# Kernel tuning notes

Measured on AMD Instinct MI355X. Metric: run time of the kernel, lower is better.

Reference implementation:

```python
import jax, jax.numpy as jnp
import numpy as np

N = 50000
E = 800000
IN_C, HID_C, OUT_C = 128, 256, 128
BN_EPS = 1e-5


def glorot(key, shape):
    fan_in, fan_out = shape
    lim = float(np.sqrt(6.0 / (fan_in + fan_out)))
    return jax.random.uniform(key, shape, jnp.float32, -lim, lim)


def setup_inputs() -> dict:
    key = jax.random.key(0)
    ks = jax.random.split(key, 16)
    inp = {
        "x": jax.random.normal(ks[0], (N, IN_C), jnp.float32),
        "edge_index": jax.random.randint(ks[1], (2, E), 0, N, jnp.int64),
        # SAGEConv 1 (in->hid): lin_l has bias, lin_r has no bias (PyG default)
        "wl1": glorot(ks[2], (IN_C, HID_C)), "bl1": jnp.zeros((HID_C,), jnp.float32),
        "wr1": glorot(ks[3], (IN_C, HID_C)),
        # SAGEConv 2 (hid->hid)
        "wl2": glorot(ks[4], (HID_C, HID_C)), "bl2": jnp.zeros((HID_C,), jnp.float32),
        "wr2": glorot(ks[5], (HID_C, HID_C)),
        # SAGEConv 3 (hid->out)
        "wl3": glorot(ks[6], (HID_C, OUT_C)), "bl3": jnp.zeros((OUT_C,), jnp.float32),
        "wr3": glorot(ks[7], (HID_C, OUT_C)),
        # BatchNorm params (eval mode: running stats)
        "bn1_w": jnp.ones((HID_C,), jnp.float32), "bn1_b": jnp.zeros((HID_C,), jnp.float32),
        "bn1_m": jax.random.normal(ks[8], (HID_C,), jnp.float32) * 0.1,
        "bn1_v": jax.random.uniform(ks[9], (HID_C,), jnp.float32, 0.5, 1.5),
        "bn2_w": jnp.ones((HID_C,), jnp.float32), "bn2_b": jnp.zeros((HID_C,), jnp.float32),
        "bn2_m": jax.random.normal(ks[10], (HID_C,), jnp.float32) * 0.1,
        "bn2_v": jax.random.uniform(ks[11], (HID_C,), jnp.float32, 0.5, 1.5),
    }
    return inp


def sage_conv(x, src, dst, wl, bl, wr):
    # mean aggregation of source-node features at destination nodes
    agg = jax.ops.segment_sum(x[src], dst, num_segments=N)          # [N, d_in]
    deg = jax.ops.segment_sum(jnp.ones((E,), x.dtype), dst, num_segments=N)
    mean = agg / jnp.maximum(deg, 1.0)[:, None]
    return mean @ wl + bl + x @ wr                                   # [N, d_out]


def batch_norm(x, w, b, m, v):
    return (x - m) * jax.lax.rsqrt(v + BN_EPS) * w + b


def reference(x, edge_index, wl1, bl1, wr1, wl2, bl2, wr2, wl3, bl3, wr3,
              bn1_w, bn1_b, bn1_m, bn1_v, bn2_w, bn2_b, bn2_m, bn2_v):
    src, dst = edge_index[0], edge_index[1]
    # layer 1: SAGEConv -> BN -> ReLU (dropout is identity in eval mode)
    h = sage_conv(x, src, dst, wl1, bl1, wr1)
    h = jax.nn.relu(batch_norm(h, bn1_w, bn1_b, bn1_m, bn1_v))
    # layer 2
    h = sage_conv(h, src, dst, wl2, bl2, wr2)
    h = jax.nn.relu(batch_norm(h, bn2_w, bn2_b, bn2_m, bn2_v))
    # output layer: plain SAGEConv
    return sage_conv(h, src, dst, wl3, bl3, wr3)
```

## Files before the change

### kernel.cpp

```cpp
#include <hip/hip_runtime.h>
#include <hip/hip_bf16.h>

#define NN 50000
#define NE 800000
#define NSB 49
#define AGG_BLOCKS 2048

typedef __attribute__((ext_vector_type(8))) short bh8;
typedef __attribute__((ext_vector_type(4))) float f32x4;

static __device__ __forceinline__ unsigned short f2bf(float f){
  unsigned u = __float_as_uint(f);
  unsigned r = (u + 0x7fffu + ((u >> 16) & 1u)) >> 16;
  return (unsigned short)r;
}
static __device__ __forceinline__ float bflo(unsigned u){ return __uint_as_float(u << 16); }
static __device__ __forceinline__ float bfhi(unsigned u){ return __uint_as_float(u & 0xffff0000u); }
static __device__ __forceinline__ unsigned packbf2(float lo, float hi){
  return ((unsigned)f2bf(hi) << 16) | (unsigned)f2bf(lo);
}

static __device__ __forceinline__ void gload16(const void* g, void* l){
  __builtin_amdgcn_global_load_lds(
      (const __attribute__((address_space(1))) unsigned int*)g,
      (__attribute__((address_space(3))) unsigned int*)l, 16, 0, 0);
}

__global__ void hist_k(const int* __restrict__ dstv, int* __restrict__ cnt,
                       int* __restrict__ rank){
  int i = blockIdx.x * 256 + threadIdx.x;
  if (i < NE) rank[i] = atomicAdd(&cnt[dstv[i]], 1);
}

__global__ __launch_bounds__(256) void scan1_k(const int* __restrict__ cnt,
                                               int* __restrict__ rowp,
                                               int* __restrict__ bsum){
  __shared__ int sa[256], sb[256];
  const int t = threadIdx.x, blk = blockIdx.x;
  const int base = blk * 1024 + t * 4;
  int4 v = make_int4(0, 0, 0, 0);
  if (base + 3 < NN) v = *reinterpret_cast<const int4*>(cnt + base);
  else if (base < NN){
    v.x = cnt[base];
    if (base + 1 < NN) v.y = cnt[base + 1];
    if (base + 2 < NN) v.z = cnt[base + 2];
  }
  const int s = v.x + v.y + v.z + v.w;
  sa[t] = s; __syncthreads();
  int* a = sa; int* b = sb;
  for (int off = 1; off < 256; off <<= 1){
    int val = a[t]; if (t >= off) val += a[t - off];
    b[t] = val; __syncthreads();
    int* tmp = a; a = b; b = tmp;
  }
  const int ex = a[t] - s;
  if (base < NN){
    rowp[base] = ex;
    if (base + 1 < NN) rowp[base + 1] = ex + v.x;
    if (base + 2 < NN) rowp[base + 2] = ex + v.x + v.y;
    if (base + 3 < NN) rowp[base + 3] = ex + v.x + v.y + v.z;
  }
  if (t == 255) bsum[blk] = a[255];
}

__global__ void scan2_k(int* __restrict__ bsum){
  __shared__ int s[64];
  const int t = threadIdx.x;
  s[t] = (t < NSB) ? bsum[t] : 0;
  __syncthreads();
  if (t == 0){
    int run = 0;
    for (int i = 0; i < NSB; ++i){ int c = s[i]; s[i] = run; run += c; }
  }
  __syncthreads();
  if (t < NSB) bsum[t] = s[t];
}

__global__ __launch_bounds__(256) void scan3_k(int* __restrict__ rowp,
                                               const int* __restrict__ bsum){
  const int blk = blockIdx.x;
  const int base = blk * 1024 + threadIdx.x * 4;
  const int off = bsum[blk];
  #pragma unroll
  for (int i = 0; i < 4; ++i){
    int idx = base + i;
    if (idx < NN) rowp[idx] += off;
  }
  if (blk == 0 && threadIdx.x == 0) rowp[NN] = NE;
}

__global__ __launch_bounds__(256) void fill_k(const int* __restrict__ srcv,
                       const int* __restrict__ dstv,
                       const int* __restrict__ rank,
                       const int* __restrict__ rowp, int* __restrict__ csrc){
  const int part  = blockIdx.x & 7;
  const int chunk = blockIdx.x >> 3;
  const int lo = part * (NN / 8);
  const int hi = lo + (NN / 8);
  const int base = chunk * (NE / 128);
  const int endi = base + (NE / 128);
  for (int i = base + threadIdx.x; i < endi; i += 256){
    int d = dstv[i];
    if (d >= lo && d < hi){
      csrc[rowp[d] + rank[i]] = srcv[i];
    }
  }
}

__global__ void f2b_k(const float4* __restrict__ x, uint2* __restrict__ xb){
  int i = blockIdx.x * 256 + threadIdx.x;
  if (i < NN * 128 / 4){
    float4 v = x[i];
    uint2 o; o.x = packbf2(v.x, v.y); o.y = packbf2(v.z, v.w);
    xb[i] = o;
  }
}

__global__ void f8conv_k(const uint4* __restrict__ h1, uint2* __restrict__ h1q){
  int i = blockIdx.x * 256 + threadIdx.x;
  if (i < NN * 256 / 8){
    uint4 v = h1[i];
    float f0 = bflo(v.x), f1 = bfhi(v.x), f2 = bflo(v.y), f3 = bfhi(v.y);
    float f4 = bflo(v.z), f5 = bfhi(v.z), f6 = bflo(v.w), f7 = bfhi(v.w);
    int w0 = 0, w1 = 0;
    w0 = __builtin_amdgcn_cvt_pk_fp8_f32(f0, f1, w0, false);
    w0 = __builtin_amdgcn_cvt_pk_fp8_f32(f2, f3, w0, true);
    w1 = __builtin_amdgcn_cvt_pk_fp8_f32(f4, f5, w1, false);
    w1 = __builtin_amdgcn_cvt_pk_fp8_f32(f6, f7, w1, true);
    uint2 o; o.x = (unsigned)w0; o.y = (unsigned)w1;
    h1q[i] = o;
  }
}

__global__ void prep_k(const float* __restrict__ wl1, const float* __restrict__ wr1,
                       const float* __restrict__ wl2, const float* __restrict__ wr2,
                       const float* __restrict__ wl3, const float* __restrict__ wr3,
                       const float* __restrict__ bl1, const float* __restrict__ bl2,
                       const float* __restrict__ bn1w, const float* __restrict__ bn1b,
                       const float* __restrict__ bn1m, const float* __restrict__ bn1v,
                       const float* __restrict__ bn2w, const float* __restrict__ bn2b,
                       const float* __restrict__ bn2m, const float* __restrict__ bn2v,
                       unsigned short* __restrict__ B1t, unsigned short* __restrict__ B2t,
                       unsigned short* __restrict__ B3t,
                       float* __restrict__ S1, float* __restrict__ T1,
                       float* __restrict__ S2, float* __restrict__ T2){
  int i = blockIdx.x * 256 + threadIdx.x;
  if (i < 65536){
    int n = i >> 8, k = i & 255;
    float v = (k < 128) ? wl1[k * 256 + n] : wr1[(k - 128) * 256 + n];
    B1t[n * 256 + k] = f2bf(v);
  } else if (i < 65536 + 131072){
    int j = i - 65536; int n = j >> 9, k = j & 511;
    float v = (k < 256) ? wl2[k * 256 + n] : wr2[(k - 256) * 256 + n];
    B2t[n * 512 + k] = f2bf(v);
  } else if (i < 65536 + 131072 + 65536){
    int j = i - (65536 + 131072); int n = j >> 8, k = j & 255;
    float v = (n < 128) ? wl3[k * 128 + n] : wr3[k * 128 + (n - 128)];
    B3t[n * 256 + k] = f2bf(v);
  } else if (i < 65536 + 131072 + 65536 + 512){
    int j = i - (65536 + 131072 + 65536);
    if (j < 256){
      float s = bn1w[j] * rsqrtf(bn1v[j] + 1e-5f);
      S1[j] = s; T1[j] = (bl1[j] - bn1m[j]) * s + bn1b[j];
    } else {
      int c = j - 256;
      float s = bn2w[c] * rsqrtf(bn2v[c] + 1e-5f);
      S2[c] = s; T2[c] = (bl2[c] - bn2m[c]) * s + bn2b[c];
    }
  }
}

__global__ __launch_bounds__(256) void agg128_k(const unsigned* __restrict__ feat, unsigned* __restrict__ out,
                         const int* __restrict__ rowp, const int* __restrict__ csrc){
  const int lane = threadIdx.x & 63;
  const int node0 = __builtin_amdgcn_readfirstlane(blockIdx.x * 4 + (threadIdx.x >> 6));
  const int nw = gridDim.x * 4;
  for (int node = node0; node < NN; node += nw){
    const int start = rowp[node], end = rowp[node + 1];
    float a0 = 0.f, a1 = 0.f, b0 = 0.f, b1 = 0.f;
    int e = start;
    for (; e + 7 < end; e += 8){
      unsigned u0 = feat[(size_t)csrc[e]     * 64 + lane];
      unsigned u1 = feat[(size_t)csrc[e + 1] * 64 + lane];
      unsigned u2 = feat[(size_t)csrc[e + 2] * 64 + lane];
      unsigned u3 = feat[(size_t)csrc[e + 3] * 64 + lane];
      unsigned u4 = feat[(size_t)csrc[e + 4] * 64 + lane];
      unsigned u5 = feat[(size_t)csrc[e + 5] * 64 + lane];
      unsigned u6 = feat[(size_t)csrc[e + 6] * 64 + lane];
      unsigned u7 = feat[(size_t)csrc[e + 7] * 64 + lane];
      a0 += bflo(u0); a1 += bfhi(u0);
      b0 += bflo(u1); b1 += bfhi(u1);
      a0 += bflo(u2); a1 += bfhi(u2);
      b0 += bflo(u3); b1 += bfhi(u3);
      a0 += bflo(u4); a1 += bfhi(u4);
      b0 += bflo(u5); b1 += bfhi(u5);
      a0 += bflo(u6); a1 += bfhi(u6);
      b0 += bflo(u7); b1 += bfhi(u7);
    }
    for (; e < end; ++e){
      unsigned u = feat[(size_t)csrc[e] * 64 + lane];
      a0 += bflo(u); a1 += bfhi(u);
    }
    int d = end - start;
    float inv = 1.f / (float)(d > 0 ? d : 1);
    out[(size_t)node * 64 + lane] = packbf2((a0 + b0) * inv, (a1 + b1) * inv);
  }
}

#define DEC8(u, x0, x1, x2, x3) { \
  x0 += __builtin_amdgcn_cvt_f32_fp8((u), 0); \
  x1 += __builtin_amdgcn_cvt_f32_fp8((u), 1); \
  x2 += __builtin_amdgcn_cvt_f32_fp8((u), 2); \
  x3 += __builtin_amdgcn_cvt_f32_fp8((u), 3); }

__global__ __launch_bounds__(256) void agg256q_k(const unsigned* __restrict__ featq, unsigned* __restrict__ out,
                         const int* __restrict__ rowp, const int* __restrict__ csrc){
  const int lane = threadIdx.x & 63;
  const int node0 = __builtin_amdgcn_readfirstlane(blockIdx.x * 4 + (threadIdx.x >> 6));
  const int nw = gridDim.x * 4;
  for (int node = node0; node < NN; node += nw){
    const int start = rowp[node], end = rowp[node + 1];
    float a0 = 0.f, a1 = 0.f, a2 = 0.f, a3 = 0.f;
    float b0 = 0.f, b1 = 0.f, b2 = 0.f, b3 = 0.f;
    int e = start;
    for (; e + 7 < end; e += 8){
      unsigned u0 = featq[(size_t)csrc[e]     * 64 + lane];
      unsigned u1 = featq[(size_t)csrc[e + 1] * 64 + lane];
      unsigned u2 = featq[(size_t)csrc[e + 2] * 64 + lane];
      unsigned u3 = featq[(size_t)csrc[e + 3] * 64 + lane];
      unsigned u4 = featq[(size_t)csrc[e + 4] * 64 + lane];
      unsigned u5 = featq[(size_t)csrc[e + 5] * 64 + lane];
      unsigned u6 = featq[(size_t)csrc[e + 6] * 64 + lane];
      unsigned u7 = featq[(size_t)csrc[e + 7] * 64 + lane];
      DEC8(u0, a0, a1, a2, a3) DEC8(u1, b0, b1, b2, b3)
      DEC8(u2, a0, a1, a2, a3) DEC8(u3, b0, b1, b2, b3)
      DEC8(u4, a0, a1, a2, a3) DEC8(u5, b0, b1, b2, b3)
      DEC8(u6, a0, a1, a2, a3) DEC8(u7, b0, b1, b2, b3)
    }
    for (; e < end; ++e){
      unsigned u = featq[(size_t)csrc[e] * 64 + lane];
      DEC8(u, a0, a1, a2, a3)
    }
    int d = end - start;
    float inv = 1.f / (float)(d > 0 ? d : 1);
    uint2 o; o.x = packbf2((a0 + b0) * inv, (a1 + b1) * inv);
    o.y = packbf2((a2 + b2) * inv, (a3 + b3) * inv);
    *reinterpret_cast<uint2*>(out + (size_t)node * 128 + lane * 2) = o;
  }
}

__global__ __launch_bounds__(256) void final_k(const unsigned* __restrict__ t, float* __restrict__ out,
                        const int* __restrict__ rowp, const int* __restrict__ csrc,
                        const float* __restrict__ bl3){
  const int lane = threadIdx.x & 63;
  const int node0 = __builtin_amdgcn_readfirstlane(blockIdx.x * 4 + (threadIdx.x >> 6));
  const int nw = gridDim.x * 4;
  for (int node = node0; node < NN; node += nw){
    const int start = rowp[node], end = rowp[node + 1];
    float a0 = 0.f, a1 = 0.f, b0 = 0.f, b1 = 0.f;
    int e = start;
    for (; e + 7 < end; e += 8){
      unsigned u0 = t[(size_t)csrc[e]     * 64 + lane];
      unsigned u1 = t[(size_t)csrc[e + 1] * 64 + lane];
      unsigned u2 = t[(size_t)csrc[e + 2] * 64 + lane];
      unsigned u3 = t[(size_t)csrc[e + 3] * 64 + lane];
      unsigned u4 = t[(size_t)csrc[e + 4] * 64 + lane];
      unsigned u5 = t[(size_t)csrc[e + 5] * 64 + lane];
      unsigned u6 = t[(size_t)csrc[e + 6] * 64 + lane];
      unsigned u7 = t[(size_t)csrc[e + 7] * 64 + lane];
      a0 += bflo(u0); a1 += bfhi(u0);
      b0 += bflo(u1); b1 += bfhi(u1);
      a0 += bflo(u2); a1 += bfhi(u2);
      b0 += bflo(u3); b1 += bfhi(u3);
      a0 += bflo(u4); a1 += bfhi(u4);
      b0 += bflo(u5); b1 += bfhi(u5);
      a0 += bflo(u6); a1 += bfhi(u6);
      b0 += bflo(u7); b1 += bfhi(u7);
    }
    for (; e < end; ++e){
      unsigned u = t[(size_t)csrc[e] * 64 + lane];
      a0 += bflo(u); a1 += bfhi(u);
    }
    int d = end - start;
    float inv = 1.f / (float)(d > 0 ? d : 1);
    float2* o = reinterpret_cast<float2*>(out + (size_t)node * 128) + lane;
    float2 v = *o;
    v.x += (a0 + b0) * inv + bl3[lane * 2];
    v.y += (a1 + b1) * inv + bl3[lane * 2 + 1];
    *o = v;
  }
}

template<int KTOT, int K0, int MODE>
__global__ __launch_bounds__(256) void gemm_k(
    const unsigned short* __restrict__ A0, const unsigned short* __restrict__ A1,
    const unsigned short* __restrict__ Bt,
    const float* __restrict__ S, const float* __restrict__ Tt,
    unsigned short* __restrict__ outB, unsigned short* __restrict__ outT,
    float* __restrict__ outF, int M)
{
  __shared__ __align__(16) unsigned char lds[49152];
  const int tid = threadIdx.x;
  const int lane = tid & 63;
  const int wv = tid >> 6;
  const int wm = wv >> 1, wn = wv & 1;

  const int nwg = gridDim.x;
  const int q = nwg >> 3, r8 = nwg & 7;
  const int xcd = blockIdx.x & 7, idx = blockIdx.x >> 3;
  const int wg = (xcd < r8) ? xcd * (q + 1) + idx : r8 * (q + 1) + (xcd - r8) * q + idx;
  const int bm = wg >> 1, bn = wg & 1;

  const int rr0 = tid >> 2,         g0 = (tid & 3) ^ ((tid >> 3) & 3);
  const int rr1 = (tid + 256) >> 2, g1 = ((tid + 256) & 3) ^ (((tid + 256) >> 3) & 3);
  int growA0 = bm * 128 + rr0; if (growA0 > M - 1) growA0 = M - 1;
  int growA1 = bm * 128 + rr1; if (growA1 > M - 1) growA1 = M - 1;
  const size_t browA0 = (size_t)(bn * 128 + rr0) * KTOT;
  const size_t browA1 = (size_t)(bn * 128 + rr1) * KTOT;

  const int l15 = lane & 15, kg = lane >> 4;
  const int slot = (kg ^ ((l15 >> 1) & 3)) * 16;

  constexpr int NT = KTOT / 32;

  auto STAGE = [&](int buf, int kt){
    const int kb = kt * 32;
    const unsigned short* Ap; int pitch, kk;
    if (KTOT == K0 || kb < K0){ Ap = A0; pitch = K0; kk = kb; }
    else { Ap = A1; pitch = KTOT - K0; kk = kb - K0; }
    unsigned char* base = lds + buf * 16384;
    gload16(Ap + (size_t)growA0 * pitch + kk + g0 * 8, base + tid * 16);
    gload16(Ap + (size_t)growA1 * pitch + kk + g1 * 8, base + 4096 + tid * 16);
    gload16(Bt + browA0 + kb + g0 * 8, base + 8192 + tid * 16);
    gload16(Bt + browA1 + kb + g1 * 8, base + 12288 + tid * 16);
  };

  f32x4 acc[4][4];
  #pragma unroll
  for (int i = 0; i < 4; ++i)
    #pragma unroll
    for (int j = 0; j < 4; ++j){ acc[i][j][0]=0.f; acc[i][j][1]=0.f; acc[i][j][2]=0.f; acc[i][j][3]=0.f; }

  STAGE(0, 0);
  if (NT > 1) STAGE(1, 1);

  int rb = 0, sb = 2;
  for (int kt = 0; kt < NT; ++kt){
    if (kt < NT - 1) asm volatile("s_waitcnt vmcnt(4)" ::: "memory");
    else             asm volatile("s_waitcnt vmcnt(0)" ::: "memory");
    __builtin_amdgcn_s_barrier();
    __builtin_amdgcn_sched_barrier(0);

    if (kt + 2 < NT){ STAGE(sb, kt + 2); sb = (sb == 2) ? 0 : sb + 1; }

    unsigned char* base = lds + rb * 16384;
    rb = (rb == 2) ? 0 : rb + 1;

    bh8 af[4], bf[4];
    #pragma unroll
    for (int mi = 0; mi < 4; ++mi){
      int rA = wm * 64 + mi * 16 + l15;
      af[mi] = *reinterpret_cast<const bh8*>(base + rA * 64 + slot);
    }
    #pragma unroll
    for (int ni = 0; ni < 4; ++ni){
      int rB = wn * 64 + ni * 16 + l15;
      bf[ni] = *reinterpret_cast<const bh8*>(base + 8192 + rB * 64 + slot);
    }
    __builtin_amdgcn_s_setprio(1);
    #pragma unroll
    for (int mi = 0; mi < 4; ++mi)
      #pragma unroll
      for (int ni = 0; ni < 4; ++ni)
        acc[mi][ni] = __builtin_amdgcn_mfma_f32_16x16x32_bf16(af[mi], bf[ni], acc[mi][ni], 0, 0, 0);
    __builtin_amdgcn_s_setprio(0);
  }

  #pragma unroll
  for (int mi = 0; mi < 4; ++mi){
    int rbase = bm * 128 + wm * 64 + mi * 16 + ((lane >> 4) << 2);
    #pragma unroll
    for (int ni = 0; ni < 4; ++ni){
      int col = bn * 128 + wn * 64 + ni * 16 + (lane & 15);
      #pragma unroll
      for (int j = 0; j < 4; ++j){
        int row = rbase + j;
        if (row < M){
          float v = acc[mi][ni][j];
          if (MODE == 0){
            v = v * S[col] + Tt[col];
            v = v > 0.f ? v : 0.f;
            outB[(size_t)row * 256 + col] = f2bf(v);
          } else {
            if (col < 128) outT[(size_t)row * 128 + col] = f2bf(v);
            else           outF[(size_t)row * 128 + (col - 128)] = v;
          }
        }
      }
    }
  }
}

extern "C" void kernel_launch(void* const* d_in, const int* in_sizes, int n_in,
                              void* d_out, int out_size, void* d_ws, size_t ws_size,
                              hipStream_t stream) {
  (void)in_sizes; (void)n_in; (void)out_size; (void)ws_size;
  const float* x   = (const float*)d_in[0];
  const int*   ei  = (const int*)d_in[1];
  const int*   srcv = ei;
  const int*   dstv = ei + NE;
  const float* wl1 = (const float*)d_in[2];
  const float* bl1 = (const float*)d_in[3];
  const float* wr1 = (const float*)d_in[4];
  const float* wl2 = (const float*)d_in[5];
  const float* bl2 = (const float*)d_in[6];
  const float* wr2 = (const float*)d_in[7];
  const float* wl3 = (const float*)d_in[8];
  const float* bl3 = (const float*)d_in[9];
  const float* wr3 = (const float*)d_in[10];
  const float* bn1w = (const float*)d_in[11];
  const float* bn1b = (const float*)d_in[12];
  const float* bn1m = (const float*)d_in[13];
  const float* bn1v = (const float*)d_in[14];
  const float* bn2w = (const float*)d_in[15];
  const float* bn2b = (const float*)d_in[16];
  const float* bn2m = (const float*)d_in[17];
  const float* bn2v = (const float*)d_in[18];

  char* ws = (char*)d_ws;
  size_t off = 0;
  auto alloc = [&](size_t bytes) -> void* {
    void* p = ws + off;
    off += (bytes + 255) & ~(size_t)255;
    return p;
  };
  int* cnt  = (int*)alloc((size_t)NN * 4);
  int* rank = (int*)alloc((size_t)NE * 4);
  int* rowp = (int*)alloc((size_t)(NN + 1) * 4);
  int* csrc = (int*)alloc((size_t)NE * 4);
  int* bsum = (int*)alloc((size_t)NSB * 4);
  unsigned short* B1t = (unsigned short*)alloc(256 * 256 * 2);
  unsigned short* B2t = (unsigned short*)alloc(256 * 512 * 2);
  unsigned short* B3t = (unsigned short*)alloc(256 * 256 * 2);
  float* S1 = (float*)alloc(256 * 4);
  float* T1 = (float*)alloc(256 * 4);
  float* S2 = (float*)alloc(256 * 4);
  float* T2 = (float*)alloc(256 * 4);
  unsigned short* xb   = (unsigned short*)alloc((size_t)NN * 128 * 2);
  unsigned short* agg1 = (unsigned short*)alloc((size_t)NN * 128 * 2);
  unsigned short* h1   = (unsigned short*)alloc((size_t)NN * 256 * 2);
  unsigned short* h2   = (unsigned short*)alloc((size_t)NN * 256 * 2);
  unsigned short* agg2 = xb;
  unsigned char*  h1q  = (unsigned char*)h2;
  unsigned short* tbuf = h1;
  float* outp = (float*)d_out;

  hipMemsetAsync(cnt, 0, (size_t)NN * 4, stream);
  hist_k<<<(NE + 255) / 256, 256, 0, stream>>>(dstv, cnt, rank);
  scan1_k<<<NSB, 256, 0, stream>>>(cnt, rowp, bsum);
  scan2_k<<<1, 64, 0, stream>>>(bsum);
  scan3_k<<<NSB, 256, 0, stream>>>(rowp, bsum);
  fill_k<<<1024, 256, 0, stream>>>(srcv, dstv, rank, rowp, csrc);
  prep_k<<<1026, 256, 0, stream>>>(wl1, wr1, wl2, wr2, wl3, wr3, bl1, bl2,
                                   bn1w, bn1b, bn1m, bn1v, bn2w, bn2b, bn2m, bn2v,
                                   B1t, B2t, B3t, S1, T1, S2, T2);
  f2b_k<<<(NN * 128 / 4 + 255) / 256, 256, 0, stream>>>((const float4*)x, (uint2*)xb);

  agg128_k<<<AGG_BLOCKS, 256, 0, stream>>>((const unsigned*)xb, (unsigned*)agg1, rowp, csrc);
  gemm_k<256, 128, 0><<<782, 256, 0, stream>>>(agg1, xb, B1t, S1, T1, h1, nullptr, nullptr, NN);
  f8conv_k<<<(NN * 256 / 8 + 255) / 256, 256, 0, stream>>>((const uint4*)h1, (uint2*)h1q);
  agg256q_k<<<AGG_BLOCKS, 256, 0, stream>>>((const unsigned*)h1q, (unsigned*)agg2, rowp, csrc);
  gemm_k<512, 256, 0><<<782, 256, 0, stream>>>(agg2, h1, B2t, S2, T2, h2, nullptr, nullptr, NN);
  gemm_k<256, 256, 1><<<782, 256, 0, stream>>>(h2, h2, B3t, nullptr, nullptr, nullptr, tbuf, outp, NN);
  final_k<<<AGG_BLOCKS, 256, 0, stream>>>((const unsigned*)tbuf, outp, rowp, csrc, bl3);
}
```

Baseline: 269.7 us.

## Quantize gather operands of all three aggregations to fp8 and fuse conversions

Layer-1 input features and the layer-3 pre-aggregation transform are now stored as fp8 rather than bf16, so the gather kernels read half the bytes per edge. The separate h1 fp8 conversion kernel is removed: the first GEMM epilogue writes fp8 h1 alongside bf16, and f2b_k emits both the bf16 and fp8 copies of x. This trades accuracy (fp8 e4m3 on raw x and on the layer-3 transform) for lower gather bandwidth and one fewer launch. The GEMM epilogue gains extra per-element byte stores.

```diff
diff --git a/kernel.cpp b/kernel.cpp
--- a/kernel.cpp
+++ b/kernel.cpp
@@ -18,6 +18,9 @@
 static __device__ __forceinline__ float bfhi(unsigned u){ return __uint_as_float(u & 0xffff0000u); }
 static __device__ __forceinline__ unsigned packbf2(float lo, float hi){
   return ((unsigned)f2bf(hi) << 16) | (unsigned)f2bf(lo);
+}
+static __device__ __forceinline__ unsigned char f2fp8(float v){
+  return (unsigned char)(__builtin_amdgcn_cvt_pk_fp8_f32(v, v, 0, false) & 0xff);
 }
 
 static __device__ __forceinline__ void gload16(const void* g, void* l){
@@ -107,28 +110,17 @@
   }
 }
 
-__global__ void f2b_k(const float4* __restrict__ x, uint2* __restrict__ xb){
+__global__ void f2b_k(const float4* __restrict__ x, uint2* __restrict__ xb,
+                      unsigned* __restrict__ xq){
   int i = blockIdx.x * 256 + threadIdx.x;
   if (i < NN * 128 / 4){
     float4 v = x[i];
     uint2 o; o.x = packbf2(v.x, v.y); o.y = packbf2(v.z, v.w);
     xb[i] = o;
-  }
-}
-
-__global__ void f8conv_k(const uint4* __restrict__ h1, uint2* __restrict__ h1q){
-  int i = blockIdx.x * 256 + threadIdx.x;
-  if (i < NN * 256 / 8){
-    uint4 v = h1[i];
-    float f0 = bflo(v.x), f1 = bfhi(v.x), f2 = bflo(v.y), f3 = bfhi(v.y);
-    float f4 = bflo(v.z), f5 = bfhi(v.z), f6 = bflo(v.w), f7 = bfhi(v.w);
-    int w0 = 0, w1 = 0;
-    w0 = __builtin_amdgcn_cvt_pk_fp8_f32(f0, f1, w0, false);
-    w0 = __builtin_amdgcn_cvt_pk_fp8_f32(f2, f3, w0, true);
-    w1 = __builtin_amdgcn_cvt_pk_fp8_f32(f4, f5, w1, false);
-    w1 = __builtin_amdgcn_cvt_pk_fp8_f32(f6, f7, w1, true);
-    uint2 o; o.x = (unsigned)w0; o.y = (unsigned)w1;
-    h1q[i] = o;
+    int w = 0;
+    w = __builtin_amdgcn_cvt_pk_fp8_f32(v.x, v.y, w, false);
+    w = __builtin_amdgcn_cvt_pk_fp8_f32(v.z, v.w, w, true);
+    xq[i] = (unsigned)w;
   }
 }
 
@@ -170,7 +162,8 @@
   }
 }
 
-__global__ __launch_bounds__(256) void agg128_k(const unsigned* __restrict__ feat, unsigned* __restrict__ out,
+__global__ __launch_bounds__(256) void agg128q_k(const unsigned short* __restrict__ featq,
+                         unsigned* __restrict__ out,
                          const int* __restrict__ rowp, const int* __restrict__ csrc){
   const int lane = threadIdx.x & 63;
   const int node0 = __builtin_amdgcn_readfirstlane(blockIdx.x * 4 + (threadIdx.x >> 6));
@@ -180,26 +173,26 @@
     float a0 = 0.f, a1 = 0.f, b0 = 0.f, b1 = 0.f;
     int e = start;
     for (; e + 7 < end; e += 8){
-      unsigned u0 = feat[(size_t)csrc[e]     * 64 + lane];
-      unsigned u1 = feat[(size_t)csrc[e + 1] * 64 + lane];
-      unsigned u2 = feat[(size_t)csrc[e + 2] * 64 + lane];
-      unsigned u3 = feat[(size_t)csrc[e + 3] * 64 + lane];
-      unsigned u4 = feat[(size_t)csrc[e + 4] * 64 + lane];
-      unsigned u5 = feat[(size_t)csrc[e + 5] * 64 + lane];
-      unsigned u6 = feat[(size_t)csrc[e + 6] * 64 + lane];
-      unsigned u7 = feat[(size_t)csrc[e + 7] * 64 + lane];
-      a0 += bflo(u0); a1 += bfhi(u0);
-      b0 += bflo(u1); b1 += bfhi(u1);
-      a0 += bflo(u2); a1 += bfhi(u2);
-      b0 += bflo(u3); b1 += bfhi(u3);
-      a0 += bflo(u4); a1 += bfhi(u4);
-      b0 += bflo(u5); b1 += bfhi(u5);
-      a0 += bflo(u6); a1 += bfhi(u6);
-      b0 += bflo(u7); b1 += bfhi(u7);
+      unsigned u0 = featq[(size_t)csrc[e]     * 64 + lane];
+      unsigned u1 = featq[(size_t)csrc[e + 1] * 64 + lane];
+      unsigned u2 = featq[(size_t)csrc[e + 2] * 64 + lane];
+      unsigned u3 = featq[(size_t)csrc[e + 3] * 64 + lane];
+      unsigned u4 = featq[(size_t)csrc[e + 4] * 64 + lane];
+      unsigned u5 = featq[(size_t)csrc[e + 5] * 64 + lane];
+      unsigned u6 = featq[(size_t)csrc[e + 6] * 64 + lane];
+      unsigned u7 = featq[(size_t)csrc[e + 7] * 64 + lane];
+      a0 += __builtin_amdgcn_cvt_f32_fp8(u0, 0); a1 += __builtin_amdgcn_cvt_f32_fp8(u0, 1);
+      b0 += __builtin_amdgcn_cvt_f32_fp8(u1, 0); b1 += __builtin_amdgcn_cvt_f32_fp8(u1, 1);
+      a0 += __builtin_amdgcn_cvt_f32_fp8(u2, 0); a1 += __builtin_amdgcn_cvt_f32_fp8(u2, 1);
+      b0 += __builtin_amdgcn_cvt_f32_fp8(u3, 0); b1 += __builtin_amdgcn_cvt_f32_fp8(u3, 1);
+      a0 += __builtin_amdgcn_cvt_f32_fp8(u4, 0); a1 += __builtin_amdgcn_cvt_f32_fp8(u4, 1);
+      b0 += __builtin_amdgcn_cvt_f32_fp8(u5, 0); b1 += __builtin_amdgcn_cvt_f32_fp8(u5, 1);
+      a0 += __builtin_amdgcn_cvt_f32_fp8(u6, 0); a1 += __builtin_amdgcn_cvt_f32_fp8(u6, 1);
+      b0 += __builtin_amdgcn_cvt_f32_fp8(u7, 0); b1 += __builtin_amdgcn_cvt_f32_fp8(u7, 1);
     }
     for (; e < end; ++e){
-      unsigned u = feat[(size_t)csrc[e] * 64 + lane];
-      a0 += bflo(u); a1 += bfhi(u);
+      unsigned u = featq[(size_t)csrc[e] * 64 + lane];
+      a0 += __builtin_amdgcn_cvt_f32_fp8(u, 0); a1 += __builtin_amdgcn_cvt_f32_fp8(u, 1);
     }
     int d = end - start;
     float inv = 1.f / (float)(d > 0 ? d : 1);
@@ -249,7 +242,7 @@
   }
 }
 
-__global__ __launch_bounds__(256) void final_k(const unsigned* __restrict__ t, float* __restrict__ out,
+__global__ __launch_bounds__(256) void final_k(const unsigned short* __restrict__ tq, float* __restrict__ out,
                         const int* __restrict__ rowp, const int* __restrict__ csrc,
                         const float* __restrict__ bl3){
   const int lane = threadIdx.x & 63;
@@ -260,26 +253,26 @@
     float a0 = 0.f, a1 = 0.f, b0 = 0.f, b1 = 0.f;
     int e = start;
     for (; e + 7 < end; e += 8){
-      unsigned u0 = t[(size_t)csrc[e]     * 64 + lane];
-      unsigned u1 = t[(size_t)csrc[e + 1] * 64 + lane];
-      unsigned u2 = t[(size_t)csrc[e + 2] * 64 + lane];
-      unsigned u3 = t[(size_t)csrc[e + 3] * 64 + lane];
-      unsigned u4 = t[(size_t)csrc[e + 4] * 64 + lane];
-      unsigned u5 = t[(size_t)csrc[e + 5] * 64 + lane];
-      unsigned u6 = t[(size_t)csrc[e + 6] * 64 + lane];
-      unsigned u7 = t[(size_t)csrc[e + 7] * 64 + lane];
-      a0 += bflo(u0); a1 += bfhi(u0);
-      b0 += bflo(u1); b1 += bfhi(u1);
-      a0 += bflo(u2); a1 += bfhi(u2);
-      b0 += bflo(u3); b1 += bfhi(u3);
-      a0 += bflo(u4); a1 += bfhi(u4);
-      b0 += bflo(u5); b1 += bfhi(u5);
-      a0 += bflo(u6); a1 += bfhi(u6);
-      b0 += bflo(u7); b1 += bfhi(u7);
+      unsigned u0 = tq[(size_t)csrc[e]     * 64 + lane];
+      unsigned u1 = tq[(size_t)csrc[e + 1] * 64 + lane];
+      unsigned u2 = tq[(size_t)csrc[e + 2] * 64 + lane];
+      unsigned u3 = tq[(size_t)csrc[e + 3] * 64 + lane];
+      unsigned u4 = tq[(size_t)csrc[e + 4] * 64 + lane];
+      unsigned u5 = tq[(size_t)csrc[e + 5] * 64 + lane];
+      unsigned u6 = tq[(size_t)csrc[e + 6] * 64 + lane];
+      unsigned u7 = tq[(size_t)csrc[e + 7] * 64 + lane];
+      a0 += __builtin_amdgcn_cvt_f32_fp8(u0, 0); a1 += __builtin_amdgcn_cvt_f32_fp8(u0, 1);
+      b0 += __builtin_amdgcn_cvt_f32_fp8(u1, 0); b1 += __builtin_amdgcn_cvt_f32_fp8(u1, 1);
+      a0 += __builtin_amdgcn_cvt_f32_fp8(u2, 0); a1 += __builtin_amdgcn_cvt_f32_fp8(u2, 1);
+      b0 += __builtin_amdgcn_cvt_f32_fp8(u3, 0); b1 += __builtin_amdgcn_cvt_f32_fp8(u3, 1);
+      a0 += __builtin_amdgcn_cvt_f32_fp8(u4, 0); a1 += __builtin_amdgcn_cvt_f32_fp8(u4, 1);
+      b0 += __builtin_amdgcn_cvt_f32_fp8(u5, 0); b1 += __builtin_amdgcn_cvt_f32_fp8(u5, 1);
+      a0 += __builtin_amdgcn_cvt_f32_fp8(u6, 0); a1 += __builtin_amdgcn_cvt_f32_fp8(u6, 1);
+      b0 += __builtin_amdgcn_cvt_f32_fp8(u7, 0); b1 += __builtin_amdgcn_cvt_f32_fp8(u7, 1);
     }
     for (; e < end; ++e){
-      unsigned u = t[(size_t)csrc[e] * 64 + lane];
-      a0 += bflo(u); a1 += bfhi(u);
+      unsigned u = tq[(size_t)csrc[e] * 64 + lane];
+      a0 += __builtin_amdgcn_cvt_f32_fp8(u, 0); a1 += __builtin_amdgcn_cvt_f32_fp8(u, 1);
     }
     int d = end - start;
     float inv = 1.f / (float)(d > 0 ? d : 1);
@@ -296,7 +289,7 @@
     const unsigned short* __restrict__ A0, const unsigned short* __restrict__ A1,
     const unsigned short* __restrict__ Bt,
     const float* __restrict__ S, const float* __restrict__ Tt,
-    unsigned short* __restrict__ outB, unsigned short* __restrict__ outT,
+    unsigned short* __restrict__ outB, unsigned char* __restrict__ outQ,
     float* __restrict__ outF, int M)
 {
   __shared__ __align__(16) unsigned char lds[49152];
@@ -391,8 +384,9 @@
             v = v * S[col] + Tt[col];
             v = v > 0.f ? v : 0.f;
             outB[(size_t)row * 256 + col] = f2bf(v);
+            if (outQ) outQ[(size_t)row * 256 + col] = f2fp8(v);
           } else {
-            if (col < 128) outT[(size_t)row * 128 + col] = f2bf(v);
+            if (col < 128) outQ[(size_t)row * 128 + col] = f2fp8(v);
             else           outF[(size_t)row * 128 + (col - 128)] = v;
           }
         }
@@ -452,7 +446,8 @@
   unsigned short* h2   = (unsigned short*)alloc((size_t)NN * 256 * 2);
   unsigned short* agg2 = xb;
   unsigned char*  h1q  = (unsigned char*)h2;
-  unsigned short* tbuf = h1;
+  unsigned*       xq   = (unsigned*)((unsigned char*)h2 + (size_t)NN * 256);
+  unsigned char*  tq   = (unsigned char*)h1;
   float* outp = (float*)d_out;
 
   hipMemsetAsync(cnt, 0, (size_t)NN * 4, stream);
@@ -464,13 +459,12 @@
   prep_k<<<1026, 256, 0, stream>>>(wl1, wr1, wl2, wr2, wl3, wr3, bl1, bl2,
                                    bn1w, bn1b, bn1m, bn1v, bn2w, bn2b, bn2m, bn2v,
                                    B1t, B2t, B3t, S1, T1, S2, T2);
-  f2b_k<<<(NN * 128 / 4 + 255) / 256, 256, 0, stream>>>((const float4*)x, (uint2*)xb);
-
-  agg128_k<<<AGG_BLOCKS, 256, 0, stream>>>((const unsigned*)xb, (unsigned*)agg1, rowp, csrc);
-  gemm_k<256, 128, 0><<<782, 256, 0, stream>>>(agg1, xb, B1t, S1, T1, h1, nullptr, nullptr, NN);
-  f8conv_k<<<(NN * 256 / 8 + 255) / 256, 256, 0, stream>>>((const uint4*)h1, (uint2*)h1q);
+  f2b_k<<<(NN * 128 / 4 + 255) / 256, 256, 0, stream>>>((const float4*)x, (uint2*)xb, xq);
+
+  agg128q_k<<<AGG_BLOCKS, 256, 0, stream>>>((const unsigned short*)xq, (unsigned*)agg1, rowp, csrc);
+  gemm_k<256, 128, 0><<<782, 256, 0, stream>>>(agg1, xb, B1t, S1, T1, h1, h1q, nullptr, NN);
   agg256q_k<<<AGG_BLOCKS, 256, 0, stream>>>((const unsigned*)h1q, (unsigned*)agg2, rowp, csrc);
   gemm_k<512, 256, 0><<<782, 256, 0, stream>>>(agg2, h1, B2t, S2, T2, h2, nullptr, nullptr, NN);
-  gemm_k<256, 256, 1><<<782, 256, 0, stream>>>(h2, h2, B3t, nullptr, nullptr, nullptr, tbuf, outp, NN);
-  final_k<<<AGG_BLOCKS, 256, 0, stream>>>((const unsigned*)tbuf, outp, rowp, csrc, bl3);
-}
+  gemm_k<256, 256, 1><<<782, 256, 0, stream>>>(h2, h2, B3t, nullptr, nullptr, nullptr, tq, outp, NN);
+  final_k<<<AGG_BLOCKS, 256, 0, stream>>>((const unsigned short*)tq, outp, rowp, csrc, bl3);
+}
```

Measured after the change: 252.3 us. 6.4% less time.
